# Kernel tuning notes

Measured on AMD Instinct MI355X. Metric: run time of the kernel, lower is better.

The kernel has to match this reference:

```python
import jax, jax.numpy as jnp
import numpy as np

B, H, O, T = 512, 1024, 256, 128  # batch, hidden_dim, output_dim, target_length


def setup_inputs() -> dict:
    key = jax.random.key(0)
    ks = jax.random.split(key, 7)
    s = 1.0 / np.sqrt(H)  # torch LSTM/Linear init range
    u = lambda k, shape: jax.random.uniform(k, shape, jnp.float32, -s, s)
    return {
        "encoder_hidden": jax.random.normal(ks[0], (B, H), jnp.float32),
        "target_length": T,
        "W_ih": u(ks[1], (4 * H, O)),   # gate order i,f,g,o (torch layout)
        "W_hh": u(ks[2], (4 * H, H)),
        "b_ih": u(ks[3], (4 * H,)),
        "b_hh": u(ks[4], (4 * H,)),
        "W_out": u(ks[5], (O, H)),
        "b_out": u(ks[6], (O,)),
    }


def reference(encoder_hidden, target_length, W_ih, W_hh, b_ih, b_hh, W_out, b_out):
    # Dropout is identity (inference). teacher_forcing=None path: feed back prediction.
    bsz = encoder_hidden.shape[0]
    out_dim = W_out.shape[0]
    h0 = encoder_hidden
    c0 = jnp.zeros_like(h0)
    x0 = jnp.zeros((bsz, out_dim), dtype=encoder_hidden.dtype)
    b = b_ih + b_hh

    def step(carry, _):
        h, c, x = carry
        gates = x @ W_ih.T + h @ W_hh.T + b          # (B, 4H)
        i, f, g, o = jnp.split(gates, 4, axis=-1)
        c = jax.nn.sigmoid(f) * c + jax.nn.sigmoid(i) * jnp.tanh(g)
        h = jax.nn.sigmoid(o) * jnp.tanh(c)
        pred = h @ W_out.T + b_out                    # (B, O)
        return (h, c, pred), pred

    _, preds = jax.lax.scan(step, (h0, c0, x0), None, length=target_length)
    return jnp.transpose(preds, (1, 0, 2))  # (B, T, O)
```

## Files before the change

### kernel.cpp

```cpp
#include <hip/hip_runtime.h>
#include <hip/hip_bf16.h>

using short8  = __attribute__((ext_vector_type(8))) short;
using floatx4 = __attribute__((ext_vector_type(4))) float;
typedef unsigned short u16;
typedef unsigned int   u32;

#define DEVINL static __device__ __forceinline__

constexpr int kB = 512;
constexpr int kH = 1024;
constexpr int kO = 256;
constexpr int kT = 128;
constexpr int kG = 4096;

DEVINL u16 f2bf(float x) {
  union { float f; unsigned u; } v; v.f = x;
  unsigned r = v.u + 0x7fffu + ((v.u >> 16) & 1u);
  return (u16)(r >> 16);
}
DEVINL float sigm(float x)  { return 1.0f / (1.0f + __expf(-x)); }
DEVINL float tanhx(float x) { return 1.0f - 2.0f / (__expf(2.0f * x) + 1.0f); }

DEVINL void gload16(const void* src, void* ldsbase) {
  __builtin_amdgcn_global_load_lds((__attribute__((address_space(1))) void*)(char*)src,
                                   (__attribute__((address_space(3))) void*)ldsbase,
                                   16, 0, 0);
}
DEVINL short8 lds8(const void* p) { return *(const short8*)p; }


__global__ void k_init(const float* __restrict__ enc, float* __restrict__ c,
                       u16* __restrict__ h0) {
  int i = blockIdx.x * 256 + threadIdx.x;
  c[i]  = 0.0f;
  h0[i] = f2bf(enc[i]);
}

__global__ void k_zbar(u32* __restrict__ bar) {
  bar[blockIdx.x * 256 + threadIdx.x] = 0u;
}

__global__ void k_bias(const float* __restrict__ bih, const float* __restrict__ bhh,
                       const float* __restrict__ Wih, const float* __restrict__ bout,
                       float* __restrict__ bias0, float* __restrict__ bias1) {
  int n = blockIdx.x * 256 + threadIdx.x;
  float b0 = bih[n] + bhh[n];
  const float* row = Wih + (long)n * 256;
  float s = 0.f;
  for (int j = 0; j < 256; ++j) s += row[j] * bout[j];
  bias0[n] = b0;
  bias1[n] = b0 + s;
}

__global__ void k_w0(const float* __restrict__ Whh, u16* __restrict__ Wt0) {
  const int r = blockIdx.x;
  const int k = threadIdx.x * 4;
  const int n = ((r >> 6) << 4) | (r & 15);
  const int g = (r >> 4) & 3;
  const float4 v = *(const float4*)(Whh + (long)(g * 1024 + n) * 1024 + k);
  ushort4 o; o.x = f2bf(v.x); o.y = f2bf(v.y); o.z = f2bf(v.z); o.w = f2bf(v.w);
  *(ushort4*)(Wt0 + (long)r * 1024 + k) = o;
}

__global__ void k_wo(const float* __restrict__ Wout, u16* __restrict__ Wob) {
  const long i = ((long)blockIdx.x * 256 + threadIdx.x) * 4;
  const float4 v = *(const float4*)(Wout + i);
  ushort4 o; o.x = f2bf(v.x); o.y = f2bf(v.y); o.z = f2bf(v.z); o.w = f2bf(v.w);
  *(ushort4*)(Wob + i) = o;
}

__global__ __launch_bounds__(256) void k_w1(
    const float* __restrict__ Wih, const float* __restrict__ Wout,
    const float* __restrict__ Whh, u16* __restrict__ Wt1) {
  __shared__ float sW[16][256];
  const int g = blockIdx.x & 3, n16 = blockIdx.x >> 2;
  const int tid = threadIdx.x;
#pragma unroll
  for (int nl = 0; nl < 16; ++nl)
    sW[nl][tid] = Wih[(long)(g * 1024 + n16 * 16 + nl) * 256 + tid];
  __syncthreads();
  const int k4 = tid * 4;
  float acc[16][4];
#pragma unroll
  for (int nl = 0; nl < 16; ++nl)
#pragma unroll
    for (int q = 0; q < 4; ++q) acc[nl][q] = 0.f;
  for (int j = 0; j < 256; ++j) {
    const float4 wo = *(const float4*)(Wout + (long)j * 1024 + k4);
#pragma unroll
    for (int nl = 0; nl < 16; ++nl) {
      const float w = sW[nl][j];
      acc[nl][0] += w * wo.x; acc[nl][1] += w * wo.y;
      acc[nl][2] += w * wo.z; acc[nl][3] += w * wo.w;
    }
  }
#pragma unroll
  for (int nl = 0; nl < 16; ++nl) {
    const int n = n16 * 16 + nl;
    const int rout = n16 * 64 + g * 16 + nl;
    const float* hh = Whh + (long)(g * 1024 + n) * 1024 + k4;
    ushort4 o;
    o.x = f2bf(hh[0] + acc[nl][0]); o.y = f2bf(hh[1] + acc[nl][1]);
    o.z = f2bf(hh[2] + acc[nl][2]); o.w = f2bf(hh[3] + acc[nl][3]);
    *(ushort4*)(Wt1 + (long)rout * 1024 + k4) = o;
  }
}

__global__ __launch_bounds__(256) void k_step(
    const u16* __restrict__ Xprev, u16* __restrict__ Hnext,
    float* __restrict__ c, const u16* __restrict__ Wt,
    const float* __restrict__ bias) {
  __shared__ u16 As[64 * 64];
  __shared__ u16 Bs[128 * 64];

  const int tid  = threadIdx.x;
  const int lane = tid & 63;
  const int wid  = tid >> 6;
  const int wr   = wid >> 1;
  const int wc   = wid & 1;
  const int n0   = blockIdx.x * 32;
  const int m0   = blockIdx.y * 64;
  const long wrow0 = (long)n0 * 4;
  const int hi  = lane >> 4;
  const int l15 = lane & 15;

  floatx4 acc[2][4];
#pragma unroll
  for (int a2 = 0; a2 < 2; ++a2)
#pragma unroll
    for (int f = 0; f < 4; ++f)
#pragma unroll
      for (int r = 0; r < 4; ++r) acc[a2][f][r] = 0.0f;

  for (int kt = 0; kt < 16; ++kt) {
    const int kb = kt * 128;
#pragma unroll
    for (int i = 0; i < 2; ++i) {
      const int u = i * 256 + tid;
      const int row = u >> 3;
      const int off = (u & 7) * 16;
      const char* src = (const char*)Xprev + ((long)(m0 + row) << 11) + kb +
                        (off ^ ((row & 7) << 4));
      gload16(src, (char*)As + (i * 256 + wid * 64) * 16);
    }
#pragma unroll
    for (int i = 0; i < 4; ++i) {
      const int u = i * 256 + tid;
      const int col = u >> 3;
      const int off = (u & 7) * 16;
      const char* src = (const char*)Wt + ((wrow0 + col) << 11) + kb +
                        (off ^ ((col & 7) << 4));
      gload16(src, (char*)Bs + (i * 256 + wid * 64) * 16);
    }
    __syncthreads();
#pragma unroll
    for (int ks = 0; ks < 2; ++ks) {
      const int kbyte = ks * 64 + hi * 16;
      const int ra = wr * 32 + l15;
      short8 a0 = lds8((const char*)As + ra * 128 + (kbyte ^ ((ra & 7) << 4)));
      const int rb = ra + 16;
      short8 a1 = lds8((const char*)As + rb * 128 + (kbyte ^ ((rb & 7) << 4)));
#pragma unroll
      for (int f = 0; f < 4; ++f) {
        const int colx = wc * 64 + f * 16 + l15;
        short8 b = lds8((const char*)Bs + colx * 128 + (kbyte ^ ((colx & 7) << 4)));
        acc[0][f] = __builtin_amdgcn_mfma_f32_16x16x32_bf16(a0, b, acc[0][f], 0, 0, 0);
        acc[1][f] = __builtin_amdgcn_mfma_f32_16x16x32_bf16(a1, b, acc[1][f], 0, 0, 0);
      }
    }
    __syncthreads();
  }

  const int n_glob = n0 + wc * 16 + l15;
  const float bi = bias[n_glob];
  const float bf = bias[1024 + n_glob];
  const float bg = bias[2048 + n_glob];
  const float bo = bias[3072 + n_glob];
#pragma unroll
  for (int a2 = 0; a2 < 2; ++a2) {
#pragma unroll
    for (int r = 0; r < 4; ++r) {
      const int row = m0 + wr * 32 + a2 * 16 + hi * 4 + r;
      const long ci = (long)row * kH + n_glob;
      const float iv = sigm(acc[a2][0][r] + bi);
      const float fv = sigm(acc[a2][1][r] + bf);
      const float gv = tanhx(acc[a2][2][r] + bg);
      const float ov = sigm(acc[a2][3][r] + bo);
      const float cn = fv * c[ci] + iv * gv;
      c[ci] = cn;
      Hnext[ci] = f2bf(ov * tanhx(cn));
    }
  }
}

__global__ __launch_bounds__(512, 2) void k_persist(
    const u16* __restrict__ Wt,
    const float* __restrict__ bias,
    const float* __restrict__ cin,
    u16* __restrict__ Hbuf,
    u32* __restrict__ bar) {
  __shared__ u16 Wlds[64 * 1024];

  const int tid = threadIdx.x;
  const int l   = tid & 63;
  const int w   = tid >> 6;
  const int l15 = l & 15;
  const int hi  = l >> 4;
  const int xcd  = blockIdx.x & 7;
  const int slot = blockIdx.x >> 3;
  const int bg   = xcd >> 1;
  const int hg   = (xcd & 1) * 32 + slot;
  const int m0   = bg * 128;
  const int myblk = blockIdx.x;
  const int pblk = ((l & 31) * 8) + (bg * 2) + (l >> 5);

  {
    const long wrow0 = (long)hg * 64;
#pragma unroll
    for (int rr = 0; rr < 16; ++rr) {
      const int u   = rr * 512 + tid;
      const int j   = u >> 8;
      const int f   = (u >> 6) & 3;
      const int h2  = (u >> 4) & 3;
      const int c15 = u & 15;
      const char* src = (const char*)Wt + ((wrow0 + f * 16 + c15) << 11) +
                        (j << 6) + (h2 << 4);
      gload16(src, (char*)Wlds + (long)u * 16);
    }
  }

  const int ncol = hg * 16 + l15;
  const float bi = bias[ncol];
  const float bf_ = bias[1024 + ncol];
  const float bg_ = bias[2048 + ncol];
  const float bo = bias[3072 + ncol];
  const int row0 = m0 + w * 16 + hi * 4;
  float creg[4];
#pragma unroll
  for (int r = 0; r < 4; ++r) creg[r] = cin[(long)(row0 + r) * kH + ncol];

  __syncthreads();

  const char* wb0 = (const char*)Wlds + (l << 4);
  const char* wb1 = wb0 + 65536;
#define BFRAG(j, f) lds8((((j) < 16) ? wb0 : wb1) + ((((j) & 15) << 12) | ((f) << 10)))

  const long arow = (long)(m0 + w * 16 + l15) * 2048 + hi * 16;
  const long HSB  = (long)kB * kH * 2;

  for (int t = 1; t < kT; ++t) {
    const char* Asrc = (const char*)Hbuf + (long)t * HSB + arow;
    floatx4 ac0 = {0.f,0.f,0.f,0.f}, ac1 = ac0, ac2 = ac0, ac3 = ac0;

    short8 bk[3][4];
#pragma unroll
    for (int g = 0; g < 3; ++g)
#pragma unroll
      for (int q = 0; q < 4; ++q)
        bk[g][q] = *(const short8*)(Asrc + ((g * 4 + q) << 6));

#pragma unroll
    for (int jg = 0; jg < 8; ++jg) {
#pragma unroll
      for (int q = 0; q < 4; ++q) {
        const int j = jg * 4 + q;
        short8 av = bk[jg % 3][q];
        ac0 = __builtin_amdgcn_mfma_f32_16x16x32_bf16(av, BFRAG(j, 0), ac0, 0, 0, 0);
        ac1 = __builtin_amdgcn_mfma_f32_16x16x32_bf16(av, BFRAG(j, 1), ac1, 0, 0, 0);
        ac2 = __builtin_amdgcn_mfma_f32_16x16x32_bf16(av, BFRAG(j, 2), ac2, 0, 0, 0);
        ac3 = __builtin_amdgcn_mfma_f32_16x16x32_bf16(av, BFRAG(j, 3), ac3, 0, 0, 0);
      }
      if (jg < 5) {
#pragma unroll
        for (int q = 0; q < 4; ++q)
          bk[jg % 3][q] = *(const short8*)(Asrc + (((jg + 3) * 4 + q) << 6));
      }
    }

    u16* Hn = (u16*)((char*)Hbuf + (long)(t + 1) * HSB);
#pragma unroll
    for (int r = 0; r < 4; ++r) {
      const float iv = sigm(ac0[r] + bi);
      const float fv = sigm(ac1[r] + bf_);
      const float gv = tanhx(ac2[r] + bg_);
      const float ov = sigm(ac3[r] + bo);
      const float cn = fv * creg[r] + iv * gv;
      creg[r] = cn;
      __hip_atomic_store(&Hn[(long)(row0 + r) * kH + ncol], f2bf(ov * tanhx(cn)),
                         __ATOMIC_RELAXED, __HIP_MEMORY_SCOPE_AGENT);
    }

    if (t < kT - 1) {
      __syncthreads();
      if (tid == 0)
        __hip_atomic_store(bar + myblk * 32, (u32)t,
                           __ATOMIC_RELAXED, __HIP_MEMORY_SCOPE_AGENT);
      if (tid < 64) {
        int guard = 0;
        while (__hip_atomic_load(bar + pblk * 32, __ATOMIC_RELAXED,
                                 __HIP_MEMORY_SCOPE_AGENT) < (u32)t) {
          __builtin_amdgcn_s_sleep(1);
          if (++guard > (1 << 20)) break;
        }
      }
      __syncthreads();
    }
  }
#undef BFRAG
}

__global__ __launch_bounds__(256) void k_pred(
    const u16* __restrict__ Hbuf, long HS, int nsl,
    const u16* __restrict__ Wob, const float* __restrict__ b_out,
    float* __restrict__ out, int t0) {
  __shared__ u16 As[64 * 64];
  __shared__ u16 Bs[128 * 64];
  const int t = t0 + blockIdx.z;
  const u16* Hm = Hbuf + (long)((t + 1) % nsl) * HS;

  const int tid = threadIdx.x, lane = tid & 63, wid = tid >> 6;
  const int wr = wid >> 1, wc = wid & 1;
  const int m0 = blockIdx.y * 64;
  const int o0 = blockIdx.x * 128;
  const int hi = lane >> 4, l15 = lane & 15;

  floatx4 acc[2][4];
#pragma unroll
  for (int a2 = 0; a2 < 2; ++a2)
#pragma unroll
    for (int f = 0; f < 4; ++f)
#pragma unroll
      for (int r = 0; r < 4; ++r) acc[a2][f][r] = 0.0f;

  for (int kt = 0; kt < 16; ++kt) {
    const int kb = kt * 128;
#pragma unroll
    for (int i = 0; i < 2; ++i) {
      const int u = i * 256 + tid;
      const int row = u >> 3;
      const int off = (u & 7) * 16;
      const char* src = (const char*)Hm + ((long)(m0 + row) << 11) + kb +
                        (off ^ ((row & 7) << 4));
      gload16(src, (char*)As + (i * 256 + wid * 64) * 16);
    }
#pragma unroll
    for (int i = 0; i < 4; ++i) {
      const int u = i * 256 + tid;
      const int col = u >> 3;
      const int off = (u & 7) * 16;
      const char* src = (const char*)Wob + ((long)(o0 + col) << 11) + kb +
                        (off ^ ((col & 7) << 4));
      gload16(src, (char*)Bs + (i * 256 + wid * 64) * 16);
    }
    __syncthreads();
#pragma unroll
    for (int ks = 0; ks < 2; ++ks) {
      const int kbyte = ks * 64 + hi * 16;
      const int ra = wr * 32 + l15;
      short8 a0 = lds8((const char*)As + ra * 128 + (kbyte ^ ((ra & 7) << 4)));
      const int rb = ra + 16;
      short8 a1 = lds8((const char*)As + rb * 128 + (kbyte ^ ((rb & 7) << 4)));
#pragma unroll
      for (int f = 0; f < 4; ++f) {
        const int colx = wc * 64 + f * 16 + l15;
        short8 b = lds8((const char*)Bs + colx * 128 + (kbyte ^ ((colx & 7) << 4)));
        acc[0][f] = __builtin_amdgcn_mfma_f32_16x16x32_bf16(a0, b, acc[0][f], 0, 0, 0);
        acc[1][f] = __builtin_amdgcn_mfma_f32_16x16x32_bf16(a1, b, acc[1][f], 0, 0, 0);
      }
    }
    __syncthreads();
  }

#pragma unroll
  for (int f = 0; f < 4; ++f) {
    const int o = o0 + wc * 64 + f * 16 + l15;
    const float bb = b_out[o];
#pragma unroll
    for (int a2 = 0; a2 < 2; ++a2)
#pragma unroll
      for (int r = 0; r < 4; ++r) {
        const int row = m0 + wr * 32 + a2 * 16 + hi * 4 + r;
        out[((long)row * kT + t) * kO + o] = acc[a2][f][r] + bb;
      }
  }
}

extern "C" void kernel_launch(void* const* d_in, const int* in_sizes, int n_in,
                              void* d_out, int out_size, void* d_ws, size_t ws_size,
                              hipStream_t stream) {
  const float* enc  = (const float*)d_in[0];
  const float* Wih  = (const float*)d_in[2];
  const float* Whh  = (const float*)d_in[3];
  const float* bih  = (const float*)d_in[4];
  const float* bhh  = (const float*)d_in[5];
  const float* Wout = (const float*)d_in[6];
  const float* bout = (const float*)d_in[7];
  float* out = (float*)d_out;
  char*  ws  = (char*)d_ws;

  size_t off = 0;
  auto take = [&](size_t bytes) {
    size_t o = off; off += (bytes + 255) & ~(size_t)255; return o;
  };
  u16*   Wt0   = (u16*)(ws + take((size_t)kG * kH * 2));
  u16*   Wt1   = (u16*)(ws + take((size_t)kG * kH * 2));
  u16*   Wob   = (u16*)(ws + take((size_t)kO * kH * 2));
  float* bias0 = (float*)(ws + take((size_t)kG * 4));
  float* bias1 = (float*)(ws + take((size_t)kG * 4));
  float* cst   = (float*)(ws + take((size_t)kB * kH * 4));
  u32*   bar   = (u32*)(ws + take(256 * 128));
  const long HS = (long)kB * kH;
  u16* Hbuf = (u16*)(ws + off);
  const size_t havail = ws_size > off ? ws_size - off : 0;
  const bool fullhist = havail >= (size_t)(kT + 1) * HS * 2;
  const int nsl = fullhist ? (kT + 1) : 2;

  k_init<<<dim3(kB * kH / 256), dim3(256), 0, stream>>>(enc, cst, Hbuf);
  k_zbar<<<dim3(32), dim3(256), 0, stream>>>(bar);
  k_bias<<<dim3(kG / 256), dim3(256), 0, stream>>>(bih, bhh, Wih, bout, bias0, bias1);
  k_w0<<<dim3(kG), dim3(256), 0, stream>>>(Whh, Wt0);
  k_wo<<<dim3(kO * kH / 1024), dim3(256), 0, stream>>>(Wout, Wob);
  k_w1<<<dim3(256), dim3(256), 0, stream>>>(Wih, Wout, Whh, Wt1);

  if (fullhist) {
    k_step<<<dim3(kH / 32, kB / 64), dim3(256), 0, stream>>>(
        Hbuf, Hbuf + HS, cst, Wt0, bias0);
    k_persist<<<dim3(256), dim3(512), 0, stream>>>(Wt1, bias1, cst, Hbuf, bar);
    k_pred<<<dim3(kO / 128, kB / 64, kT), dim3(256), 0, stream>>>(
        Hbuf, HS, nsl, Wob, bout, out, 0);
  } else {
    for (int t = 0; t < kT; ++t) {
      const u16* Xp = Hbuf + (long)(t % nsl) * HS;
      u16*       Hn = Hbuf + (long)((t + 1) % nsl) * HS;
      k_step<<<dim3(kH / 32, kB / 64), dim3(256), 0, stream>>>(
          Xp, Hn, cst, t == 0 ? Wt0 : Wt1, t == 0 ? bias0 : bias1);
      k_pred<<<dim3(kO / 128, kB / 64, 1), dim3(256), 0, stream>>>(
          Hbuf, HS, nsl, Wob, bout, out, t);
    }
  }
}
```

Baseline: 1.456 ms.

## Switch persistent LSTM recurrence to 32x32x16 MFMA with LDS gate exchange

Replaces the per-wave 16x16x32 MFMA tiling (four gate accumulators per wave) with 32x32x16 MFMAs, where each wave computes a 32-row by 32-column tile covering two gates. Even and odd K steps go to two accumulators to hide MFMA latency. Because one thread no longer holds all four gates, the pointwise LSTM update stages accumulators through a new LDS buffer in two halves, separated by extra barriers. The aim is fewer MFMA instructions and fewer LDS B-fragment reads per step. The cost is added LDS traffic and synchronisation on the serial per-timestep critical path.

Result: slower. 2.369 ms (+62.6%).

```diff
diff --git a/kernel.cpp b/kernel.cpp
--- a/kernel.cpp
+++ b/kernel.cpp
@@ -1,8 +1,9 @@
 #include <hip/hip_runtime.h>
 #include <hip/hip_bf16.h>
 
-using short8  = __attribute__((ext_vector_type(8))) short;
-using floatx4 = __attribute__((ext_vector_type(4))) float;
+using short8   = __attribute__((ext_vector_type(8))) short;
+using floatx4  = __attribute__((ext_vector_type(4))) float;
+using floatx16 = __attribute__((ext_vector_type(16))) float;
 typedef unsigned short u16;
 typedef unsigned int   u32;
 
@@ -200,13 +201,16 @@
     const float* __restrict__ cin,
     u16* __restrict__ Hbuf,
     u32* __restrict__ bar) {
-  __shared__ u16 Wlds[64 * 1024];
+  __shared__ u16  Wlds[64 * 1024];
+  __shared__ float E[64 * 16 * 4];
 
   const int tid = threadIdx.x;
   const int l   = tid & 63;
   const int w   = tid >> 6;
-  const int l15 = l & 15;
-  const int hi  = l >> 4;
+  const int rt  = w >> 1;
+  const int ct  = w & 1;
+  const int col = l & 31;
+  const int hi  = l >> 5;
   const int xcd  = blockIdx.x & 7;
   const int slot = blockIdx.x >> 3;
   const int bg   = xcd >> 1;
@@ -220,75 +224,99 @@
 #pragma unroll
     for (int rr = 0; rr < 16; ++rr) {
       const int u   = rr * 512 + tid;
-      const int j   = u >> 8;
-      const int f   = (u >> 6) & 3;
-      const int h2  = (u >> 4) & 3;
-      const int c15 = u & 15;
-      const char* src = (const char*)Wt + ((wrow0 + f * 16 + c15) << 11) +
-                        (j << 6) + (h2 << 4);
+      const int ctu = u >> 12;
+      const int ju  = (u >> 6) & 63;
+      const int hiu = (u >> 5) & 1;
+      const int cu  = u & 31;
+      const char* src = (const char*)Wt + ((wrow0 + ctu * 32 + cu) << 11) +
+                        (ju << 5) + (hiu << 4);
       gload16(src, (char*)Wlds + (long)u * 16);
     }
   }
 
-  const int ncol = hg * 16 + l15;
-  const float bi = bias[ncol];
+  const int hid = tid & 15;
+  const int rp  = tid >> 4;
+  const int ncol = hg * 16 + hid;
+  const float bi  = bias[ncol];
   const float bf_ = bias[1024 + ncol];
   const float bg_ = bias[2048 + ncol];
-  const float bo = bias[3072 + ncol];
-  const int row0 = m0 + w * 16 + hi * 4;
+  const float bo  = bias[3072 + ncol];
   float creg[4];
 #pragma unroll
-  for (int r = 0; r < 4; ++r) creg[r] = cin[(long)(row0 + r) * kH + ncol];
+  for (int hp = 0; hp < 2; ++hp)
+#pragma unroll
+    for (int p = 0; p < 2; ++p)
+      creg[hp * 2 + p] = cin[(long)(m0 + hp * 64 + rp * 2 + p) * kH + ncol];
 
   __syncthreads();
 
-  const char* wb0 = (const char*)Wlds + (l << 4);
-  const char* wb1 = wb0 + 65536;
-#define BFRAG(j, f) lds8((((j) < 16) ? wb0 : wb1) + ((((j) & 15) << 12) | ((f) << 10)))
-
-  const long arow = (long)(m0 + w * 16 + l15) * 2048 + hi * 16;
-  const long HSB  = (long)kB * kH * 2;
+  const char* Bb = (const char*)Wlds + ct * 65536 + l * 16;
+  const long HSB   = (long)kB * kH * 2;
+  const long abase = (long)(m0 + rt * 32 + col) * 2048 + hi * 16;
 
   for (int t = 1; t < kT; ++t) {
-    const char* Asrc = (const char*)Hbuf + (long)t * HSB + arow;
-    floatx4 ac0 = {0.f,0.f,0.f,0.f}, ac1 = ac0, ac2 = ac0, ac3 = ac0;
-
-    short8 bk[3][4];
-#pragma unroll
-    for (int g = 0; g < 3; ++g)
-#pragma unroll
-      for (int q = 0; q < 4; ++q)
-        bk[g][q] = *(const short8*)(Asrc + ((g * 4 + q) << 6));
-
-#pragma unroll
-    for (int jg = 0; jg < 8; ++jg) {
-#pragma unroll
-      for (int q = 0; q < 4; ++q) {
-        const int j = jg * 4 + q;
-        short8 av = bk[jg % 3][q];
-        ac0 = __builtin_amdgcn_mfma_f32_16x16x32_bf16(av, BFRAG(j, 0), ac0, 0, 0, 0);
-        ac1 = __builtin_amdgcn_mfma_f32_16x16x32_bf16(av, BFRAG(j, 1), ac1, 0, 0, 0);
-        ac2 = __builtin_amdgcn_mfma_f32_16x16x32_bf16(av, BFRAG(j, 2), ac2, 0, 0, 0);
-        ac3 = __builtin_amdgcn_mfma_f32_16x16x32_bf16(av, BFRAG(j, 3), ac3, 0, 0, 0);
-      }
-      if (jg < 5) {
-#pragma unroll
-        for (int q = 0; q < 4; ++q)
-          bk[jg % 3][q] = *(const short8*)(Asrc + (((jg + 3) * 4 + q) << 6));
-      }
-    }
+    const char* Asrc = (const char*)Hbuf + (long)t * HSB + abase;
+    floatx16 accE, accO;
+#pragma unroll
+    for (int r = 0; r < 16; ++r) { accE[r] = 0.f; accO[r] = 0.f; }
+
+    short8 bank[2][8];
+#pragma unroll
+    for (int b = 0; b < 2; ++b)
+#pragma unroll
+      for (int q = 0; q < 8; ++q)
+        bank[b][q] = *(const short8*)(Asrc + ((b * 8 + q) << 5));
+
+#pragma unroll
+    for (int jb = 0; jb < 8; ++jb) {
+#pragma unroll
+      for (int q = 0; q < 8; ++q) {
+        const int j = jb * 8 + q;
+        short8 bfrag = lds8(Bb + j * 1024);
+        if ((q & 1) == 0)
+          accE = __builtin_amdgcn_mfma_f32_32x32x16_bf16(bank[jb & 1][q], bfrag, accE, 0, 0, 0);
+        else
+          accO = __builtin_amdgcn_mfma_f32_32x32x16_bf16(bank[jb & 1][q], bfrag, accO, 0, 0, 0);
+      }
+      if (jb < 6) {
+#pragma unroll
+        for (int q = 0; q < 8; ++q)
+          bank[jb & 1][q] = *(const short8*)(Asrc + (((jb + 2) * 8 + q) << 5));
+      }
+    }
+#pragma unroll
+    for (int r = 0; r < 16; ++r) accE[r] += accO[r];
 
     u16* Hn = (u16*)((char*)Hbuf + (long)(t + 1) * HSB);
-#pragma unroll
-    for (int r = 0; r < 4; ++r) {
-      const float iv = sigm(ac0[r] + bi);
-      const float fv = sigm(ac1[r] + bf_);
-      const float gv = tanhx(ac2[r] + bg_);
-      const float ov = sigm(ac3[r] + bo);
-      const float cn = fv * creg[r] + iv * gv;
-      creg[r] = cn;
-      __hip_atomic_store(&Hn[(long)(row0 + r) * kH + ncol], f2bf(ov * tanhx(cn)),
-                         __ATOMIC_RELAXED, __HIP_MEMORY_SCOPE_AGENT);
+    const int gate = ct * 2 + (col >> 4);
+    const int hh   = col & 15;
+
+#pragma unroll
+    for (int hp = 0; hp < 2; ++hp) {
+      __syncthreads();
+      if ((rt >> 1) == hp) {
+#pragma unroll
+        for (int r = 0; r < 16; ++r) {
+          const int row64 = (rt & 1) * 32 + (r & 3) + 8 * (r >> 2) + 4 * hi;
+          E[(row64 * 16 + hh) * 4 + gate] = accE[r];
+        }
+      }
+      __syncthreads();
+#pragma unroll
+      for (int p = 0; p < 2; ++p) {
+        const int r64 = rp * 2 + p;
+        const float4 g4 = *(const float4*)&E[(r64 * 16 + hid) * 4];
+        const float iv = sigm(g4.x + bi);
+        const float fv = sigm(g4.y + bf_);
+        const float gv = tanhx(g4.z + bg_);
+        const float ov = sigm(g4.w + bo);
+        const int ci = hp * 2 + p;
+        const float cn = fv * creg[ci] + iv * gv;
+        creg[ci] = cn;
+        __hip_atomic_store(&Hn[(long)(m0 + hp * 64 + r64) * kH + ncol],
+                           f2bf(ov * tanhx(cn)),
+                           __ATOMIC_RELAXED, __HIP_MEMORY_SCOPE_AGENT);
+      }
     }
 
     if (t < kT - 1) {
@@ -307,7 +335,6 @@
       __syncthreads();
     }
   }
-#undef BFRAG
 }
 
 __global__ __launch_bounds__(256) void k_pred(
```
